# Optimization experiments

Hardware: AMD Instinct MI355X
Metric: run time of the kernel (lower is better)

## Reference

```python
import jax, jax.numpy as jnp
import numpy as np

EPS = 1e-5
NUM_GROUPS = 8


def group_norm(x, gamma, beta):
    # x: [B, C, T]; normalize per group over (C/G, T)
    B, C, T = x.shape
    G = NUM_GROUPS
    xg = x.reshape(B, G, C // G, T)
    mean = xg.mean(axis=(2, 3), keepdims=True)
    var = xg.var(axis=(2, 3), keepdims=True)
    xn = ((xg - mean) * jax.lax.rsqrt(var + EPS)).reshape(B, C, T)
    return xn * gamma[None, :, None] + beta[None, :, None]


def mish(x):
    return x * jnp.tanh(jax.nn.softplus(x))


def setup_inputs() -> dict:
    key = jax.random.key(0)
    ks = jax.random.split(key, 7)
    C, Cb, B, T = 1024, 256, 64, 512
    # conv1d kernel_size=1 weights stored as [out, in]
    w_down = jax.random.normal(ks[0], (Cb, C), dtype=jnp.float32) / np.sqrt(C)
    b_down = jax.random.normal(ks[1], (Cb,), dtype=jnp.float32) * 0.01
    w_up = jax.random.normal(ks[2], (C, Cb), dtype=jnp.float32) / np.sqrt(Cb)
    b_up = jax.random.normal(ks[3], (C,), dtype=jnp.float32) * 0.01
    gamma = jnp.ones((C,), dtype=jnp.float32)
    beta = jnp.zeros((C,), dtype=jnp.float32)
    x = jax.random.normal(ks[4], (B, C, T), dtype=jnp.float32)
    return {"x": x, "gamma": gamma, "beta": beta,
            "w_down": w_down, "b_down": b_down,
            "w_up": w_up, "b_up": b_up}


def reference(x, gamma, beta, w_down, b_down, w_up, b_up):
    residual = x
    h = group_norm(x, gamma, beta)                       # [B, C, T]
    h = jnp.einsum('bct,oc->bot', h, w_down) + b_down[None, :, None]  # [B, Cb, T]
    h = mish(h)
    h = jnp.einsum('bct,oc->bot', h, w_up) + b_up[None, :, None]      # [B, C, T]
    return h + residual
```

## Files before the change

kernel.cpp:

```cpp
#include <hip/hip_runtime.h>
#include <hip/hip_bf16.h>
#include <stddef.h>

#define B_   64
#define C_   1024
#define CB_  256
#define T_   512
#define G_   8
#define N_   32768
#define EPS_ 1e-5f

using short8 = __attribute__((ext_vector_type(8))) short;
using f32x4  = __attribute__((ext_vector_type(4))) float;

__device__ __forceinline__ short f2bf(float f) {
    unsigned u = __float_as_uint(f);
    u += 0x7fffu + ((u >> 16) & 1u);
    return (short)(u >> 16);
}

__device__ __forceinline__ float mish_f(float y) {
    float u = __expf(fminf(y, 30.f));
    float w = u * u + 2.f * u;
    return y * (w / (w + 2.f));
}

__global__ void prep_weights(const float* __restrict__ wd, const float* __restrict__ wu,
                             short* __restrict__ wdb, short* __restrict__ wub) {
    int i = blockIdx.x * 256 + threadIdx.x;
    if (i < CB_ * C_) {
        wdb[i] = f2bf(wd[i]);
        wub[i] = f2bf(wu[i]);
    }
}

__global__ void stats_kernel(const float* __restrict__ x, const float* __restrict__ gamma,
                             const float* __restrict__ beta,
                             float* __restrict__ scaleW, float* __restrict__ shiftW) {
    const int tid = threadIdx.x;
    const int bg = blockIdx.x;
    const int b = bg >> 3, g = bg & 7;
    const float4* p = (const float4*)(x + ((size_t)b * C_ + g * 128) * T_);
    float s = 0.f, q = 0.f;
    for (int i = tid; i < 16384; i += 256) {
        float4 v = p[i];
        s += v.x + v.y + v.z + v.w;
        q += v.x * v.x + v.y * v.y + v.z * v.z + v.w * v.w;
    }
    for (int o = 32; o > 0; o >>= 1) {
        s += __shfl_down(s, o);
        q += __shfl_down(q, o);
    }
    __shared__ float red[8];
    __shared__ float mr[2];
    const int wid = tid >> 6, lane = tid & 63;
    if (lane == 0) { red[wid] = s; red[4 + wid] = q; }
    __syncthreads();
    if (tid == 0) {
        float S = red[0] + red[1] + red[2] + red[3];
        float Q = red[4] + red[5] + red[6] + red[7];
        float mean = S * (1.f / 65536.f);
        float var = Q * (1.f / 65536.f) - mean * mean;
        mr[0] = mean;
        mr[1] = rsqrtf(var + EPS_);
    }
    __syncthreads();
    float mean = mr[0], rstd = mr[1];
    if (tid < 128) {
        int c = g * 128 + tid;
        float sc = rstd * gamma[c];
        scaleW[b * C_ + c] = sc;
        shiftW[b * C_ + c] = beta[c] - mean * sc;
    }
}

#define LDSTR 40

__global__ __launch_bounds__(512, 2) void gemm1_mish(
    const float* __restrict__ x, const short* __restrict__ wd,
    const float* __restrict__ b_down,
    const float* __restrict__ scaleW, const float* __restrict__ shiftW,
    short* __restrict__ mid) {
    __shared__ short As[256 * LDSTR];
    __shared__ short Bs[128 * LDSTR];
    __shared__ float sS[C_], sT[C_];

    const int tid = threadIdx.x;
    const int n0 = blockIdx.x * 128;
    const int b  = n0 >> 9;

    for (int i = tid; i < C_; i += 512) {
        sS[i] = scaleW[b * C_ + i];
        sT[i] = shiftW[b * C_ + i];
    }

    const int a_kc = tid & 3;
    const int a_m  = tid >> 2;
    const int b_n  = tid & 127;
    const int b_kg = tid >> 7;
    const int wid  = tid >> 6;
    const int lane = tid & 63;
    const int wm = wid >> 1, wn = wid & 1;
    const int q = lane >> 4, l16 = lane & 15;

    f32x4 acc[4][4];
#pragma unroll
    for (int i = 0; i < 4; i++)
#pragma unroll
        for (int j = 0; j < 4; j++) acc[i][j] = 0.f;

    const float* xb = x + (size_t)b * C_ * T_ + (n0 & 511);

    short8 a0, a1;
    float bv[8];
    {
        const short* src = wd + a_m * C_ + a_kc * 8;
        a0 = *(const short8*)src;
        a1 = *(const short8*)(src + 128 * C_);
        const float* xp = xb + (size_t)(b_kg * 8) * T_ + b_n;
#pragma unroll
        for (int i = 0; i < 8; i++) bv[i] = xp[(size_t)i * T_];
    }
    __syncthreads();
    {
        *(short8*)&As[a_m * LDSTR + a_kc * 8] = a0;
        *(short8*)&As[(a_m + 128) * LDSTR + a_kc * 8] = a1;
        short8 v;
        const int kb = b_kg * 8;
#pragma unroll
        for (int i = 0; i < 8; i++) v[i] = f2bf(bv[i] * sS[kb + i] + sT[kb + i]);
        *(short8*)&Bs[b_n * LDSTR + kb] = v;
    }
    __syncthreads();

    for (int kt = 0; kt < 32; ++kt) {
        if (kt < 31) {
            const int k1 = (kt + 1) * 32;
            const short* src = wd + a_m * C_ + k1 + a_kc * 8;
            a0 = *(const short8*)src;
            a1 = *(const short8*)(src + 128 * C_);
            const float* xp = xb + (size_t)(k1 + b_kg * 8) * T_ + b_n;
#pragma unroll
            for (int i = 0; i < 8; i++) bv[i] = xp[(size_t)i * T_];
        }
        short8 af[4], bfr[4];
#pragma unroll
        for (int i = 0; i < 4; i++)
            af[i] = *(const short8*)&As[(wm * 64 + i * 16 + l16) * LDSTR + q * 8];
#pragma unroll
        for (int j = 0; j < 4; j++)
            bfr[j] = *(const short8*)&Bs[(wn * 64 + j * 16 + l16) * LDSTR + q * 8];
#pragma unroll
        for (int i = 0; i < 4; i++)
#pragma unroll
            for (int j = 0; j < 4; j++)
                acc[i][j] = __builtin_amdgcn_mfma_f32_16x16x32_bf16(af[i], bfr[j], acc[i][j], 0, 0, 0);
        __syncthreads();
        if (kt < 31) {
            *(short8*)&As[a_m * LDSTR + a_kc * 8] = a0;
            *(short8*)&As[(a_m + 128) * LDSTR + a_kc * 8] = a1;
            short8 v;
            const int kb = (kt + 1) * 32 + b_kg * 8;
            const int kl = b_kg * 8;
#pragma unroll
            for (int i = 0; i < 8; i++) v[i] = f2bf(bv[i] * sS[kb + i] + sT[kb + i]);
            *(short8*)&Bs[b_n * LDSTR + kl] = v;
        }
        __syncthreads();
    }

#pragma unroll
    for (int i = 0; i < 4; i++) {
        const int o_b = wm * 64 + i * 16 + q * 4;
#pragma unroll
        for (int j = 0; j < 4; j++) {
            const int n = n0 + wn * 64 + j * 16 + l16;
#pragma unroll
            for (int r = 0; r < 4; r++) {
                const int o = o_b + r;
                float y = acc[i][j][r] + b_down[o];
                mid[(size_t)o * N_ + n] = f2bf(mish_f(y));
            }
        }
    }
}

__global__ __launch_bounds__(256, 2) void gemm2_resid(
    const short* __restrict__ mid, const short* __restrict__ wu,
    const float* __restrict__ b_up, const float* __restrict__ x,
    float* __restrict__ out) {
    __shared__ short As[128 * LDSTR];
    __shared__ short Bs[128 * LDSTR];

    const int tid = threadIdx.x;
    const int m0 = blockIdx.x * 128;
    const int n0 = blockIdx.y * 128;

    const int a_kc = tid & 3;
    const int a_m  = tid >> 2;
    const int b_np = tid & 63;
    const int b_kg = tid >> 6;
    const int wid  = tid >> 6;
    const int lane = tid & 63;
    const int wm = wid >> 1, wn = wid & 1;
    const int q = lane >> 4, l16 = lane & 15;

    f32x4 acc[4][4];
#pragma unroll
    for (int i = 0; i < 4; i++)
#pragma unroll
        for (int j = 0; j < 4; j++) acc[i][j] = 0.f;

    short8 a0, a1;
    ushort2 bv[8];
    {
        const short* src = wu + (m0 + a_m) * CB_ + a_kc * 8;
        a0 = *(const short8*)src;
        a1 = *(const short8*)(src + 64 * CB_);
        const unsigned short* mp = (const unsigned short*)mid + (size_t)(b_kg * 8) * N_ + n0 + b_np * 2;
#pragma unroll
        for (int i = 0; i < 8; i++) bv[i] = *(const ushort2*)(mp + (size_t)i * N_);
    }
    {
        *(short8*)&As[a_m * LDSTR + a_kc * 8] = a0;
        *(short8*)&As[(a_m + 64) * LDSTR + a_kc * 8] = a1;
        short8 v0, v1;
#pragma unroll
        for (int i = 0; i < 8; i++) { v0[i] = (short)bv[i].x; v1[i] = (short)bv[i].y; }
        *(short8*)&Bs[(b_np * 2) * LDSTR + b_kg * 8] = v0;
        *(short8*)&Bs[(b_np * 2 + 1) * LDSTR + b_kg * 8] = v1;
    }
    __syncthreads();

    for (int kt = 0; kt < 8; ++kt) {
        if (kt < 7) {
            const int k1 = (kt + 1) * 32;
            const short* src = wu + (m0 + a_m) * CB_ + k1 + a_kc * 8;
            a0 = *(const short8*)src;
            a1 = *(const short8*)(src + 64 * CB_);
            const unsigned short* mp = (const unsigned short*)mid + (size_t)(k1 + b_kg * 8) * N_ + n0 + b_np * 2;
#pragma unroll
            for (int i = 0; i < 8; i++) bv[i] = *(const ushort2*)(mp + (size_t)i * N_);
        }
        short8 af[4], bfr[4];
#pragma unroll
        for (int i = 0; i < 4; i++)
            af[i] = *(const short8*)&As[(wm * 64 + i * 16 + l16) * LDSTR + q * 8];
#pragma unroll
        for (int j = 0; j < 4; j++)
            bfr[j] = *(const short8*)&Bs[(wn * 64 + j * 16 + l16) * LDSTR + q * 8];
#pragma unroll
        for (int i = 0; i < 4; i++)
#pragma unroll
            for (int j = 0; j < 4; j++)
                acc[i][j] = __builtin_amdgcn_mfma_f32_16x16x32_bf16(af[i], bfr[j], acc[i][j], 0, 0, 0);
        __syncthreads();
        if (kt < 7) {
            *(short8*)&As[a_m * LDSTR + a_kc * 8] = a0;
            *(short8*)&As[(a_m + 64) * LDSTR + a_kc * 8] = a1;
            short8 v0, v1;
#pragma unroll
            for (int i = 0; i < 8; i++) { v0[i] = (short)bv[i].x; v1[i] = (short)bv[i].y; }
            *(short8*)&Bs[(b_np * 2) * LDSTR + b_kg * 8] = v0;
            *(short8*)&Bs[(b_np * 2 + 1) * LDSTR + b_kg * 8] = v1;
        }
        __syncthreads();
    }

    const int b = n0 >> 9;
    const int t0 = n0 & 511;
#pragma unroll
    for (int i = 0; i < 4; i++) {
        const int c_b = m0 + wm * 64 + i * 16 + q * 4;
#pragma unroll
        for (int j = 0; j < 4; j++) {
            const int tt = t0 + wn * 64 + j * 16 + l16;
#pragma unroll
            for (int r = 0; r < 4; r++) {
                const int c = c_b + r;
                const size_t gi = ((size_t)b * C_ + c) * T_ + tt;
                out[gi] = acc[i][j][r] + b_up[c] + x[gi];
            }
        }
    }
}

extern "C" void kernel_launch(void* const* d_in, const int* in_sizes, int n_in,
                              void* d_out, int out_size, void* d_ws, size_t ws_size,
                              hipStream_t stream) {
    const float* x      = (const float*)d_in[0];
    const float* gamma  = (const float*)d_in[1];
    const float* beta   = (const float*)d_in[2];
    const float* w_down = (const float*)d_in[3];
    const float* b_down = (const float*)d_in[4];
    const float* w_up   = (const float*)d_in[5];
    const float* b_up   = (const float*)d_in[6];
    float* out = (float*)d_out;

    float* scaleW = (float*)d_ws;
    float* shiftW = scaleW + B_ * C_;
    short* wdb    = (short*)(shiftW + B_ * C_);
    short* wub    = wdb + CB_ * C_;
    short* mid    = wub + C_ * CB_;

    prep_weights<<<dim3((CB_ * C_ + 255) / 256), 256, 0, stream>>>(w_down, w_up, wdb, wub);
    stats_kernel<<<dim3(B_ * G_), 256, 0, stream>>>(x, gamma, beta, scaleW, shiftW);
    gemm1_mish<<<dim3(N_ / 128), 512, 0, stream>>>(x, wdb, b_down, scaleW, shiftW, mid);
    gemm2_resid<<<dim3(C_ / 128, N_ / 128), 256, 0, stream>>>(mid, wub, b_up, x, out);
}
```

Measured before the change: 330.7 us.

## Fuse up-projection GEMM into down-projection kernel, keeping mish activations in LDS

Merges the two GEMM kernels so each 128-column block computes the down-projection plus mish, stores the bf16 activations in shared memory, then runs the up-projection over all 1024 output channels in two halves. This removes the global round trip for the intermediate tensor and one kernel launch. The up-projection weights are pre-swizzled into an MFMA-fragment layout so they can be loaded straight from global memory into registers without LDS staging. The cost is much more LDS per block (about 67 KB for Ms), which may lower occupancy. Each block now also carries the full up-projection, with 128 accumulator registers per thread and weights re-read from L2 by every block.

```diff
diff --git a/kernel.cpp b/kernel.cpp
--- a/kernel.cpp
+++ b/kernel.cpp
@@ -10,8 +10,9 @@
 #define N_   32768
 #define EPS_ 1e-5f
 
-using short8 = __attribute__((ext_vector_type(8))) short;
-using f32x4  = __attribute__((ext_vector_type(4))) float;
+using short8  = __attribute__((ext_vector_type(8))) short;
+using short4v = __attribute__((ext_vector_type(4))) short;
+using f32x4   = __attribute__((ext_vector_type(4))) float;
 
 __device__ __forceinline__ short f2bf(float f) {
     unsigned u = __float_as_uint(f);
@@ -26,11 +27,14 @@
 }
 
 __global__ void prep_weights(const float* __restrict__ wd, const float* __restrict__ wu,
-                             short* __restrict__ wdb, short* __restrict__ wub) {
+                             short* __restrict__ wdb, short* __restrict__ wut) {
     int i = blockIdx.x * 256 + threadIdx.x;
     if (i < CB_ * C_) {
         wdb[i] = f2bf(wd[i]);
-        wub[i] = f2bf(wu[i]);
+        int m = i >> 8, k = i & 255;
+        int idx = (((m >> 4) * 8 + (k >> 5)) << 9) + (((k >> 3) & 3) << 7)
+                + ((m & 15) << 3) + (k & 7);
+        wut[idx] = f2bf(wu[i]);
     }
 }
 
@@ -75,19 +79,23 @@
 }
 
 #define LDSTR 40
-
-__global__ __launch_bounds__(512, 2) void gemm1_mish(
+#define MSTR  264
+
+__global__ __launch_bounds__(512, 2) void fused_adapter(
     const float* __restrict__ x, const short* __restrict__ wd,
     const float* __restrict__ b_down,
     const float* __restrict__ scaleW, const float* __restrict__ shiftW,
-    short* __restrict__ mid) {
+    const short* __restrict__ wut, const float* __restrict__ b_up,
+    float* __restrict__ out) {
     __shared__ short As[256 * LDSTR];
     __shared__ short Bs[128 * LDSTR];
     __shared__ float sS[C_], sT[C_];
+    __shared__ short Ms[128 * MSTR];
 
     const int tid = threadIdx.x;
     const int n0 = blockIdx.x * 128;
     const int b  = n0 >> 9;
+    const int t0 = n0 & 511;
 
     for (int i = tid; i < C_; i += 512) {
         sS[i] = scaleW[b * C_ + i];
@@ -109,7 +117,7 @@
 #pragma unroll
         for (int j = 0; j < 4; j++) acc[i][j] = 0.f;
 
-    const float* xb = x + (size_t)b * C_ * T_ + (n0 & 511);
+    const float* xb = x + (size_t)b * C_ * T_ + t0;
 
     short8 a0, a1;
     float bv[8];
@@ -172,114 +180,63 @@
 #pragma unroll
     for (int i = 0; i < 4; i++) {
         const int o_b = wm * 64 + i * 16 + q * 4;
+        const float bd0 = b_down[o_b];
+        const float bd1 = b_down[o_b + 1];
+        const float bd2 = b_down[o_b + 2];
+        const float bd3 = b_down[o_b + 3];
 #pragma unroll
         for (int j = 0; j < 4; j++) {
-            const int n = n0 + wn * 64 + j * 16 + l16;
-#pragma unroll
-            for (int r = 0; r < 4; r++) {
-                const int o = o_b + r;
-                float y = acc[i][j][r] + b_down[o];
-                mid[(size_t)o * N_ + n] = f2bf(mish_f(y));
-            }
-        }
-    }
-}
-
-__global__ __launch_bounds__(256, 2) void gemm2_resid(
-    const short* __restrict__ mid, const short* __restrict__ wu,
-    const float* __restrict__ b_up, const float* __restrict__ x,
-    float* __restrict__ out) {
-    __shared__ short As[128 * LDSTR];
-    __shared__ short Bs[128 * LDSTR];
-
-    const int tid = threadIdx.x;
-    const int m0 = blockIdx.x * 128;
-    const int n0 = blockIdx.y * 128;
-
-    const int a_kc = tid & 3;
-    const int a_m  = tid >> 2;
-    const int b_np = tid & 63;
-    const int b_kg = tid >> 6;
-    const int wid  = tid >> 6;
-    const int lane = tid & 63;
-    const int wm = wid >> 1, wn = wid & 1;
-    const int q = lane >> 4, l16 = lane & 15;
-
-    f32x4 acc[4][4];
-#pragma unroll
-    for (int i = 0; i < 4; i++)
-#pragma unroll
-        for (int j = 0; j < 4; j++) acc[i][j] = 0.f;
-
-    short8 a0, a1;
-    ushort2 bv[8];
-    {
-        const short* src = wu + (m0 + a_m) * CB_ + a_kc * 8;
-        a0 = *(const short8*)src;
-        a1 = *(const short8*)(src + 64 * CB_);
-        const unsigned short* mp = (const unsigned short*)mid + (size_t)(b_kg * 8) * N_ + n0 + b_np * 2;
-#pragma unroll
-        for (int i = 0; i < 8; i++) bv[i] = *(const ushort2*)(mp + (size_t)i * N_);
-    }
-    {
-        *(short8*)&As[a_m * LDSTR + a_kc * 8] = a0;
-        *(short8*)&As[(a_m + 64) * LDSTR + a_kc * 8] = a1;
-        short8 v0, v1;
-#pragma unroll
-        for (int i = 0; i < 8; i++) { v0[i] = (short)bv[i].x; v1[i] = (short)bv[i].y; }
-        *(short8*)&Bs[(b_np * 2) * LDSTR + b_kg * 8] = v0;
-        *(short8*)&Bs[(b_np * 2 + 1) * LDSTR + b_kg * 8] = v1;
-    }
-    __syncthreads();
-
-    for (int kt = 0; kt < 8; ++kt) {
-        if (kt < 7) {
-            const int k1 = (kt + 1) * 32;
-            const short* src = wu + (m0 + a_m) * CB_ + k1 + a_kc * 8;
-            a0 = *(const short8*)src;
-            a1 = *(const short8*)(src + 64 * CB_);
-            const unsigned short* mp = (const unsigned short*)mid + (size_t)(k1 + b_kg * 8) * N_ + n0 + b_np * 2;
-#pragma unroll
-            for (int i = 0; i < 8; i++) bv[i] = *(const ushort2*)(mp + (size_t)i * N_);
-        }
-        short8 af[4], bfr[4];
+            const int nl = wn * 64 + j * 16 + l16;
+            short4v v;
+            v[0] = f2bf(mish_f(acc[i][j][0] + bd0));
+            v[1] = f2bf(mish_f(acc[i][j][1] + bd1));
+            v[2] = f2bf(mish_f(acc[i][j][2] + bd2));
+            v[3] = f2bf(mish_f(acc[i][j][3] + bd3));
+            *(short4v*)&Ms[nl * MSTR + o_b] = v;
+        }
+    }
+    __syncthreads();
+
+#pragma unroll 1
+    for (int half = 0; half < 2; ++half) {
+        f32x4 a2[4][8];
 #pragma unroll
         for (int i = 0; i < 4; i++)
-            af[i] = *(const short8*)&As[(wm * 64 + i * 16 + l16) * LDSTR + q * 8];
-#pragma unroll
-        for (int j = 0; j < 4; j++)
-            bfr[j] = *(const short8*)&Bs[(wn * 64 + j * 16 + l16) * LDSTR + q * 8];
-#pragma unroll
-        for (int i = 0; i < 4; i++)
-#pragma unroll
-            for (int j = 0; j < 4; j++)
-                acc[i][j] = __builtin_amdgcn_mfma_f32_16x16x32_bf16(af[i], bfr[j], acc[i][j], 0, 0, 0);
-        __syncthreads();
-        if (kt < 7) {
-            *(short8*)&As[a_m * LDSTR + a_kc * 8] = a0;
-            *(short8*)&As[(a_m + 64) * LDSTR + a_kc * 8] = a1;
-            short8 v0, v1;
-#pragma unroll
-            for (int i = 0; i < 8; i++) { v0[i] = (short)bv[i].x; v1[i] = (short)bv[i].y; }
-            *(short8*)&Bs[(b_np * 2) * LDSTR + b_kg * 8] = v0;
-            *(short8*)&Bs[(b_np * 2 + 1) * LDSTR + b_kg * 8] = v1;
-        }
-        __syncthreads();
-    }
-
-    const int b = n0 >> 9;
-    const int t0 = n0 & 511;
-#pragma unroll
-    for (int i = 0; i < 4; i++) {
-        const int c_b = m0 + wm * 64 + i * 16 + q * 4;
-#pragma unroll
-        for (int j = 0; j < 4; j++) {
-            const int tt = t0 + wn * 64 + j * 16 + l16;
-#pragma unroll
-            for (int r = 0; r < 4; r++) {
-                const int c = c_b + r;
-                const size_t gi = ((size_t)b * C_ + c) * T_ + tt;
-                out[gi] = acc[i][j][r] + b_up[c] + x[gi];
+#pragma unroll
+            for (int j = 0; j < 8; j++) a2[i][j] = 0.f;
+
+        const int mbb = half * 32 + wid * 4;
+#pragma unroll 2
+        for (int kt = 0; kt < 8; ++kt) {
+            short8 af[4], bf2[8];
+#pragma unroll
+            for (int i = 0; i < 4; i++)
+                af[i] = *(const short8*)(wut + ((size_t)((mbb + i) * 8 + kt) << 9) + lane * 8);
+#pragma unroll
+            for (int j = 0; j < 8; j++)
+                bf2[j] = *(const short8*)&Ms[(j * 16 + l16) * MSTR + kt * 32 + q * 8];
+#pragma unroll
+            for (int i = 0; i < 4; i++)
+#pragma unroll
+                for (int j = 0; j < 8; j++)
+                    a2[i][j] = __builtin_amdgcn_mfma_f32_16x16x32_bf16(af[i], bf2[j], a2[i][j], 0, 0, 0);
+        }
+
+#pragma unroll
+        for (int i = 0; i < 4; i++) {
+            const int c_b = half * 512 + wid * 64 + i * 16 + q * 4;
+            const float bu0 = b_up[c_b];
+            const float bu1 = b_up[c_b + 1];
+            const float bu2 = b_up[c_b + 2];
+            const float bu3 = b_up[c_b + 3];
+#pragma unroll
+            for (int j = 0; j < 8; j++) {
+                const int tt = t0 + j * 16 + l16;
+                const size_t gi = ((size_t)b * C_ + c_b) * T_ + tt;
+                out[gi]              = a2[i][j][0] + bu0 + x[gi];
+                out[gi + T_]         = a2[i][j][1] + bu1 + x[gi + T_];
+                out[gi + 2 * T_]     = a2[i][j][2] + bu2 + x[gi + 2 * T_];
+                out[gi + 3 * T_]     = a2[i][j][3] + bu3 + x[gi + 3 * T_];
             }
         }
     }
@@ -300,11 +257,10 @@
     float* scaleW = (float*)d_ws;
     float* shiftW = scaleW + B_ * C_;
     short* wdb    = (short*)(shiftW + B_ * C_);
-    short* wub    = wdb + CB_ * C_;
-    short* mid    = wub + C_ * CB_;
-
-    prep_weights<<<dim3((CB_ * C_ + 255) / 256), 256, 0, stream>>>(w_down, w_up, wdb, wub);
+    short* wut    = wdb + CB_ * C_;
+
+    prep_weights<<<dim3((CB_ * C_ + 255) / 256), 256, 0, stream>>>(w_down, w_up, wdb, wut);
     stats_kernel<<<dim3(B_ * G_), 256, 0, stream>>>(x, gamma, beta, scaleW, shiftW);
-    gemm1_mish<<<dim3(N_ / 128), 512, 0, stream>>>(x, wdb, b_down, scaleW, shiftW, mid);
-    gemm2_resid<<<dim3(C_ / 128, N_ / 128), 256, 0, stream>>>(mid, wub, b_up, x, out);
-}
+    fused_adapter<<<dim3(N_ / 128), 512, 0, stream>>>(x, wdb, b_down, scaleW, shiftW,
+                                                      wut, b_up, out);
+}
```

Result: faster. 317.4 us (-4.0%).
